# Kernel tuning notes

Hardware: AMD Instinct MI355X
Metric: run time of the kernel (lower is better)

The kernel has to match this reference:

```python
import jax, jax.numpy as jnp
import numpy as np

EPS = 1e-6
ROPE_THETA = 10000.0


def rms_norm(x, w):
    # x: [..., hd]
    var = jnp.mean(x * x, axis=-1, keepdims=True)
    return x * jax.lax.rsqrt(var + EPS) * w


def apply_rope(x):
    # x: [B, L, nH, hd], rotate-half RoPE over sequence positions
    B, L, nH, hd = x.shape
    half = hd // 2
    inv_freq = 1.0 / (ROPE_THETA ** (jnp.arange(half, dtype=jnp.float32) / half))
    pos = jnp.arange(L, dtype=jnp.float32)
    freqs = pos[:, None] * inv_freq[None, :]          # [L, half]
    cos = jnp.cos(freqs)[None, :, None, :]            # [1, L, 1, half]
    sin = jnp.sin(freqs)[None, :, None, :]
    x1, x2 = x[..., :half], x[..., half:]
    return jnp.concatenate([x1 * cos - x2 * sin, x1 * sin + x2 * cos], axis=-1)


def setup_inputs() -> dict:
    key = jax.random.key(0)
    ks = jax.random.split(key, 5)
    B, H, W, C = 2, 48, 48, 512
    nH, nKV = 8, 4
    hd = C // nH
    s = 0.02
    return {
        "x": jax.random.normal(ks[0], (B, H, W, C), jnp.float32),
        "wq": jax.random.normal(ks[1], (C, C), jnp.float32) * s,
        "wk": jax.random.normal(ks[2], (C, nKV * hd), jnp.float32) * s,
        "wv": jax.random.normal(ks[3], (C, nKV * hd), jnp.float32) * s,
        "wo": jax.random.normal(ks[4], (C, C), jnp.float32) * s,
        "q_norm_w": jnp.ones((hd,), jnp.float32),
        "k_norm_w": jnp.ones((hd,), jnp.float32),
    }


def reference(x, wq, wk, wv, wo, q_norm_w, k_norm_w):
    B, H, W, C = x.shape
    L = H * W
    nH = 8
    hd = C // nH
    nKV = wk.shape[-1] // hd

    xf = x.reshape(B, L, C)
    q = (xf @ wq).reshape(B, L, nH, hd)
    k = (xf @ wk).reshape(B, L, nKV, hd)
    v = (xf @ wv).reshape(B, L, nKV, hd)

    q = apply_rope(rms_norm(q, q_norm_w))
    k = apply_rope(rms_norm(k, k_norm_w))

    q = q.transpose(0, 2, 1, 3)                       # [B, nH, L, hd]
    k = k.transpose(0, 2, 1, 3)                       # [B, nKV, L, hd]
    v = v.transpose(0, 2, 1, 3)
    if nKV < nH:
        rep = nH // nKV
        k = jnp.repeat(k, rep, axis=1)                # repeat_interleave over heads
        v = jnp.repeat(v, rep, axis=1)

    scale = 1.0 / jnp.sqrt(jnp.array(hd, jnp.float32))
    scores = jnp.einsum("bhqd,bhkd->bhqk", q, k) * scale
    attn = jax.nn.softmax(scores, axis=-1)
    out = jnp.einsum("bhqk,bhkd->bhqd", attn, v)      # [B, nH, L, hd]
    out = out.transpose(0, 2, 1, 3).reshape(B, H, W, C)
    return out @ wo
```

## Files before the change

### kernel.cpp

```cpp
#include <hip/hip_runtime.h>
#include <cstdint>
#include <cmath>

typedef float    f32x4  __attribute__((ext_vector_type(4)));
typedef uint32_t u32x4  __attribute__((ext_vector_type(4)));
typedef uint16_t u16x8  __attribute__((ext_vector_type(8)));
typedef __bf16   bf16x8 __attribute__((ext_vector_type(8)));

#define DEVI __device__ __forceinline__

#if __has_builtin(__builtin_amdgcn_exp2f)
DEVI float fast_exp2(float x) { return __builtin_amdgcn_exp2f(x); }
#else
DEVI float fast_exp2(float x) { return exp2f(x); }
#endif

constexpr int L   = 2304;
constexpr int C   = 512;
constexpr int NH  = 8;
constexpr int NKV = 4;
constexpr int HD  = 64;
constexpr int Bn  = 2;
constexpr int M   = Bn * L;
constexpr int NQKV = C + 2 * NKV * HD;
constexpr int NSPLIT = 4;
constexpr int KTILES = 36 / NSPLIT;

constexpr int LDP = 72;

DEVI uint16_t f2bf(float f) {
  union { float f; uint32_t u; } v; v.f = f;
  uint32_t u = v.u;
  return (uint16_t)((u + 0x7fffu + ((u >> 16) & 1u)) >> 16);
}
DEVI float bf2f(uint16_t h) {
  union { uint32_t u; float f; } v; v.u = ((uint32_t)h) << 16;
  return v.f;
}
DEVI uint16_t f2h(float f) {
  _Float16 h = (_Float16)f;
  return __builtin_bit_cast(uint16_t, h);
}
DEVI float h2f(uint16_t u) {
  return (float)__builtin_bit_cast(_Float16, u);
}

DEVI bool detect_fp32(const void* qw_raw) {
  return ((const uint16_t*)qw_raw)[0] == 0;
}

DEVI f32x4 mfma_bf16(u32x4 a, u32x4 b, f32x4 c) {
  return __builtin_amdgcn_mfma_f32_16x16x32_bf16(
      __builtin_bit_cast(bf16x8, a), __builtin_bit_cast(bf16x8, b), c, 0, 0, 0);
}

DEVI void gld16(const void* g, void* l) {
  __builtin_amdgcn_global_load_lds((const __attribute__((address_space(1))) void*)g,
                                   (__attribute__((address_space(3))) void*)l,
                                   16, 0, 0);
}

__global__ __launch_bounds__(256) void k_prep(
    const void* __restrict__ x,
    const void* __restrict__ wq, const void* __restrict__ wk,
    const void* __restrict__ wv, const void* __restrict__ wo,
    const void* __restrict__ qw_raw,
    uint16_t* __restrict__ xb,
    uint16_t* __restrict__ wqkvT, uint16_t* __restrict__ woT) {
  const bool f32 = detect_fp32(qw_raw);
  const int bi = blockIdx.x;
  const int t = threadIdx.x;
  if (bi >= 192) {
    const int i = ((bi - 192) * 256 + t) * 8;
    if (f32) {
      const float* xf = (const float*)x;
      const f32x4 v0 = *(const f32x4*)&xf[i];
      const f32x4 v1 = *(const f32x4*)&xf[i + 4];
      u16x8 o;
#pragma unroll
      for (int j = 0; j < 4; ++j) { o[j] = f2bf(v0[j]); o[j + 4] = f2bf(v1[j]); }
      *(u16x8*)&xb[i] = o;
    } else {
      *(u16x8*)&xb[i] = *(const u16x8*)((const uint16_t*)x + i);
    }
    return;
  }
  __shared__ uint16_t tile[64][72];
  const void* src; uint16_t* dst;
  int src_ld, col0, n0, k0;
  if (bi < 128) {
    const int nt = bi & 15, kt = bi >> 4;
    n0 = nt * 64; k0 = kt * 64;
    if (n0 < 512)      { src = wq; src_ld = 512; col0 = n0; }
    else if (n0 < 768) { src = wk; src_ld = 256; col0 = n0 - 512; }
    else               { src = wv; src_ld = 256; col0 = n0 - 768; }
    dst = wqkvT + n0 * 512 + k0;
  } else {
    const int bi2 = bi - 128;
    const int nt = bi2 & 7, kt = bi2 >> 3;
    n0 = nt * 64; k0 = kt * 64;
    src = wo; src_ld = 512; col0 = n0;
    dst = woT + n0 * 512 + k0;
  }
  const int rr = t >> 2, c4 = t & 3;
  if (f32) {
    const float* s32 = (const float*)src;
    for (int cc = c4; cc < 8; cc += 4) {
      const f32x4 v0 = *(const f32x4*)&s32[(k0 + rr) * src_ld + col0 + cc * 8];
      const f32x4 v1 = *(const f32x4*)&s32[(k0 + rr) * src_ld + col0 + cc * 8 + 4];
      for (int j = 0; j < 4; ++j) {
        tile[rr][cc * 8 + j]     = f2bf(v0[j]);
        tile[rr][cc * 8 + j + 4] = f2bf(v1[j]);
      }
    }
  } else {
    const uint16_t* s16 = (const uint16_t*)src;
    for (int cc = c4; cc < 8; cc += 4) {
      const u16x8 v = *(const u16x8*)&s16[(k0 + rr) * src_ld + col0 + cc * 8];
      for (int j = 0; j < 8; ++j) tile[rr][cc * 8 + j] = v[j];
    }
  }
  __syncthreads();
  for (int cc = c4; cc < 8; cc += 4) {
    u16x8 o;
    for (int j = 0; j < 8; ++j) o[j] = tile[cc * 8 + j][rr];
    *(u16x8*)&dst[rr * 512 + cc * 8] = o;
  }
}

DEVI void gemm128_core(const uint16_t* __restrict__ A, const uint16_t* __restrict__ Bt,
                       int m0, int n0, uint16_t* As, uint16_t* Bs, f32x4 acc[4][4]) {
  const int t = threadIdx.x;
  const int lane = t & 63, wave = t >> 6;
  const int l15 = lane & 15, quad = lane >> 4;
  const int wm = wave >> 1, wn = wave & 1;
#pragma unroll
  for (int i = 0; i < 4; ++i)
#pragma unroll
    for (int j = 0; j < 4; ++j) acc[i][j] = f32x4{0.f, 0.f, 0.f, 0.f};

  for (int k0 = 0; k0 < C; k0 += 64) {
    __syncthreads();
#pragma unroll
    for (int rr = 0; rr < 4; ++rr) {
      const int slotbase = rr * 256 + wave * 64;
      const int slot = slotbase + lane;
      const int row = slot >> 3;
      const int ch = (slot & 7) ^ (row & 7);
      gld16(&A [(m0 + row) * C + k0 + ch * 8], &As[slotbase * 8]);
      gld16(&Bt[(n0 + row) * C + k0 + ch * 8], &Bs[slotbase * 8]);
    }
    __syncthreads();
#pragma unroll
    for (int ks = 0; ks < 2; ++ks) {
      const int c = ks * 4 + quad;
      u32x4 af[4], bf[4];
#pragma unroll
      for (int mt = 0; mt < 4; ++mt) {
        const int r = wm * 64 + mt * 16 + l15;
        af[mt] = *(const u32x4*)&As[r * 64 + (c ^ (r & 7)) * 8];
      }
#pragma unroll
      for (int nt = 0; nt < 4; ++nt) {
        const int r = wn * 64 + nt * 16 + l15;
        bf[nt] = *(const u32x4*)&Bs[r * 64 + (c ^ (r & 7)) * 8];
      }
#pragma unroll
      for (int mt = 0; mt < 4; ++mt)
#pragma unroll
        for (int nt = 0; nt < 4; ++nt)
          acc[mt][nt] = mfma_bf16(af[mt], bf[nt], acc[mt][nt]);
    }
  }
}

__global__ __launch_bounds__(256, 2) void k_gemm_qkv(
    const uint16_t* __restrict__ xb, const uint16_t* __restrict__ wqkvT,
    uint16_t* __restrict__ q_p, uint16_t* __restrict__ k_p, uint16_t* __restrict__ v_t,
    const void* __restrict__ qw_raw, const void* __restrict__ kw_raw) {
  __shared__ uint16_t As[128 * 64], Bs[128 * 64];
  const bool f32 = detect_fp32(qw_raw);
  const int m0 = blockIdx.x * 128, n0 = blockIdx.y * 128;
  f32x4 acc[4][4];
  gemm128_core(xb, wqkvT, m0, n0, As, Bs, acc);
  const int t = threadIdx.x, lane = t & 63, wave = t >> 6;
  const int l15 = lane & 15, quad = lane >> 4;
  const int wm = wave >> 1, wn = wave & 1;
  const int col0 = n0 + wn * 64;

  if (col0 < C + NKV * HD) {
    const bool isq = (col0 < C);
    const void* wr = isq ? qw_raw : kw_raw;
    float w4[4];
#pragma unroll
    for (int nt = 0; nt < 4; ++nt)
      w4[nt] = f32 ? ((const float*)wr)[nt * 16 + l15]
                   : bf2f(((const uint16_t*)wr)[nt * 16 + l15]);
    const float cfreq = -0.41524101186092f;
    const float f0 = fast_exp2((float)l15 * cfreq);
    const float f1 = fast_exp2((float)(16 + l15) * cfreq);
    float sF0, cF0, sF1, cF1;
    sincosf(f0, &sF0, &cF0);
    sincosf(f1, &sF1, &cF1);
    const float sc = isq ? 0.125f * 1.44269504088896f : 1.0f;
    const int head = isq ? (col0 >> 6) : ((col0 - C) >> 6);
    uint16_t* plane = isq ? q_p : k_p;
    const int nheads = isq ? NH : NKV;
#pragma unroll
    for (int mt = 0; mt < 4; ++mt) {
      const int gm = m0 + wm * 64 + mt * 16 + quad * 4;
      const int b = gm / L;
      const int l = gm - b * L;
      uint16_t* dst = plane + ((b * nheads + head) * L + l) * HD + l15;
      float s0, c0, s1, c1;
      sincosf((float)l * f0, &s0, &c0);
      sincosf((float)l * f1, &s1, &c1);
#pragma unroll
      for (int r = 0; r < 4; ++r) {
        float x0 = acc[mt][0][r], x1 = acc[mt][1][r];
        float x2 = acc[mt][2][r], x3 = acc[mt][3][r];
        float ss = x0 * x0 + x1 * x1 + x2 * x2 + x3 * x3;
        ss += __shfl_xor(ss, 1, 64); ss += __shfl_xor(ss, 2, 64);
        ss += __shfl_xor(ss, 4, 64); ss += __shfl_xor(ss, 8, 64);
        const float inv = 1.0f / sqrtf(ss * (1.0f / 64.0f) + 1e-6f);
        x0 *= inv * w4[0]; x1 *= inv * w4[1]; x2 *= inv * w4[2]; x3 *= inv * w4[3];
        dst[r * HD +  0] = f2bf((x0 * c0 - x2 * s0) * sc);
        dst[r * HD + 16] = f2bf((x1 * c1 - x3 * s1) * sc);
        dst[r * HD + 32] = f2bf((x0 * s0 + x2 * c0) * sc);
        dst[r * HD + 48] = f2bf((x1 * s1 + x3 * c1) * sc);
        const float ns0 = s0 * cF0 + c0 * sF0, nc0 = c0 * cF0 - s0 * sF0;
        const float ns1 = s1 * cF1 + c1 * sF1, nc1 = c1 * cF1 - s1 * sF1;
        s0 = ns0; c0 = nc0; s1 = ns1; c1 = nc1;
      }
    }
  } else {
    const int vh = (col0 - C - NKV * HD) >> 6;
#pragma unroll
    for (int mt = 0; mt < 4; ++mt) {
      const int gm = m0 + wm * 64 + mt * 16 + quad * 4;
      const int b = gm / L;
      const int l = gm - b * L;
#pragma unroll
      for (int nt = 0; nt < 4; ++nt) {
        uint16_t* dst = v_t + ((b * NKV + vh) * HD + nt * 16 + l15) * L + l;
#pragma unroll
        for (int r = 0; r < 4; ++r) dst[r] = f2bf(acc[mt][nt][r]);
      }
    }
  }
}

__global__ __launch_bounds__(256, 3) void k_attn(
    const uint16_t* __restrict__ q_p, const uint16_t* __restrict__ k_p,
    const uint16_t* __restrict__ v_t,
    uint16_t* __restrict__ Ohat, float* __restrict__ lpart) {
  __shared__ uint16_t Ks[2][4096], Vs[4096];
  __shared__ uint16_t Ps[4][48 * LDP];
  const int t = threadIdx.x, lane = t & 63, wave = t >> 6;
  const int l15 = lane & 15, quad = lane >> 4;

  const int bid = blockIdx.x;
  const int s   = bid / 192;
  const int rem = bid - s * 192;
  const int bkvh = rem / 24;
  const int qg   = rem - bkvh * 24;
  const int b = bkvh >> 2, kvh = bkvh & 3;
  const int u = qg * 4 + wave;
  const int h_local = u / 48;
  const int qt = u - h_local * 48;
  const int bh = b * NH + kvh * 2 + h_local;
  const int q0 = qt * 48;

  const uint16_t* qbase = q_p + (bh * L + q0) * HD;
  const uint16_t* kbase = k_p + (b * NKV + kvh) * L * HD;
  const uint16_t* vbase = v_t + (b * NKV + kvh) * HD * L;
  const int kstart = s * KTILES * 64;

  u32x4 qf[3][2];
#pragma unroll
  for (int mt = 0; mt < 3; ++mt)
#pragma unroll
    for (int ks = 0; ks < 2; ++ks)
      qf[mt][ks] = *(const u32x4*)&qbase[(mt * 16 + l15) * HD + (ks * 4 + quad) * 8];

  f32x4 O[3][4];
  float lp[3][4];
#pragma unroll
  for (int mt = 0; mt < 3; ++mt) {
#pragma unroll
    for (int nt = 0; nt < 4; ++nt) O[mt][nt] = f32x4{0.f, 0.f, 0.f, 0.f};
#pragma unroll
    for (int r = 0; r < 4; ++r) lp[mt][r] = 0.f;
  }

  uint16_t* Pw = Ps[wave];

  auto stageK = [&](int key0, int buf) {
#pragma unroll
    for (int rr = 0; rr < 2; ++rr) {
      const int slotbase = rr * 256 + wave * 64;
      const int slot = slotbase + lane;
      const int row = slot >> 3, cs = slot & 7;
      const int ch = cs ^ (row & 7);
      gld16(&kbase[(key0 + row) * HD + ch * 8], &Ks[buf][slotbase * 8]);
    }
  };
  auto stageV = [&](int key0) {
#pragma unroll
    for (int rr = 0; rr < 2; ++rr) {
      const int slotbase = rr * 256 + wave * 64;
      const int slot = slotbase + lane;
      const int row = slot >> 3, cs = slot & 7;
      const int ch = cs ^ (row & 7);
      gld16(&vbase[row * L + key0 + ch * 8], &Vs[slotbase * 8]);
    }
  };

  stageK(kstart, 0);

#pragma unroll 1
  for (int kb = 0; kb < KTILES; ++kb) {
    const int cur = kb & 1;
    __syncthreads();
    stageV(kstart + kb * 64);
    if (kb + 1 < KTILES) stageK(kstart + (kb + 1) * 64, cur ^ 1);

#pragma unroll
    for (int nt = 0; nt < 4; ++nt) {
      f32x4 S[3];
#pragma unroll
      for (int mt = 0; mt < 3; ++mt) S[mt] = f32x4{0.f, 0.f, 0.f, 0.f};
      const int kr = nt * 16 + l15;
#pragma unroll
      for (int ks = 0; ks < 2; ++ks) {
        const int ch = ks * 4 + quad;
        const u32x4 kf = *(const u32x4*)&Ks[cur][(kr * 8 + (ch ^ (kr & 7))) * 8];
        __builtin_amdgcn_s_setprio(1);
#pragma unroll
        for (int mt = 0; mt < 3; ++mt)
          S[mt] = mfma_bf16(qf[mt][ks], kf, S[mt]);
        __builtin_amdgcn_s_setprio(0);
      }
#pragma unroll
      for (int mt = 0; mt < 3; ++mt)
#pragma unroll
        for (int r = 0; r < 4; ++r) {
          const float p = fast_exp2(S[mt][r]);
          lp[mt][r] += p;
          Pw[(mt * 16 + quad * 4 + r) * LDP + nt * 16 + l15] = f2bf(p);
        }
    }

    __syncthreads();

#pragma unroll
    for (int ks = 0; ks < 2; ++ks) {
      const int ch = ks * 4 + quad;
      u32x4 pf[3];
#pragma unroll
      for (int mt = 0; mt < 3; ++mt)
        pf[mt] = *(const u32x4*)&Pw[(mt * 16 + l15) * LDP + ch * 8];
#pragma unroll
      for (int nt = 0; nt < 4; ++nt) {
        const int dr = nt * 16 + l15;
        const u32x4 vf = *(const u32x4*)&Vs[(dr * 8 + (ch ^ (dr & 7))) * 8];
        __builtin_amdgcn_s_setprio(1);
#pragma unroll
        for (int mt = 0; mt < 3; ++mt)
          O[mt][nt] = mfma_bf16(pf[mt], vf, O[mt][nt]);
        __builtin_amdgcn_s_setprio(0);
      }
    }
  }

  const int obase = (s * 16 + bh) * L + q0;
#pragma unroll
  for (int mt = 0; mt < 3; ++mt)
#pragma unroll
    for (int r = 0; r < 4; ++r) {
      float lv = lp[mt][r];
#pragma unroll
      for (int m = 1; m < 16; m <<= 1) lv += __shfl_xor(lv, m, 64);
      const float rl = 1.0f / lv;
      const int row = obase + mt * 16 + quad * 4 + r;
      if (l15 == 0) lpart[row] = lv;
#pragma unroll
      for (int nt = 0; nt < 4; ++nt)
        Ohat[row * HD + nt * 16 + l15] = f2h(O[mt][nt][r] * rl);
    }
}

__global__ __launch_bounds__(256) void k_combine(
    const uint16_t* __restrict__ Ohat, const float* __restrict__ lpart,
    uint16_t* __restrict__ attn) {
  const int idx8 = blockIdx.x * 256 + threadIdx.x;
  const int row = idx8 >> 3, d0 = (idx8 & 7) * 8;
  float o[8] = {0.f, 0.f, 0.f, 0.f, 0.f, 0.f, 0.f, 0.f};
  float l = 0.f;
#pragma unroll
  for (int s = 0; s < NSPLIT; ++s) {
    const float ls = lpart[s * 16 * L + row];
    const u16x8 v = *(const u16x8*)&Ohat[(s * 16 * L + row) * HD + d0];
#pragma unroll
    for (int j = 0; j < 8; ++j) o[j] += h2f(v[j]) * ls;
    l += ls;
  }
  const int bh = row / L, lq = row - bh * L;
  const int b = bh >> 3, h = bh & 7;
  const float rl = 1.0f / l;
  u16x8 ov;
#pragma unroll
  for (int j = 0; j < 8; ++j) ov[j] = f2bf(o[j] * rl);
  *(u16x8*)&attn[(b * L + lq) * C + h * HD + d0] = ov;
}

__global__ __launch_bounds__(256, 2) void k_gemm_out(
    const uint16_t* __restrict__ attn, const uint16_t* __restrict__ woT,
    void* __restrict__ out, const void* __restrict__ qw_raw) {
  __shared__ uint16_t As[128 * 64], Bs[128 * 64];
  const bool f32 = detect_fp32(qw_raw);
  const int m0 = blockIdx.x * 128, n0 = blockIdx.y * 128;
  f32x4 acc[4][4];
  gemm128_core(attn, woT, m0, n0, As, Bs, acc);
  const int t = threadIdx.x, lane = t & 63, wave = t >> 6;
  const int l15 = lane & 15, quad = lane >> 4;
  const int wm = wave >> 1, wn = wave & 1;
#pragma unroll
  for (int mt = 0; mt < 4; ++mt) {
    const int gm = m0 + wm * 64 + mt * 16 + quad * 4;
#pragma unroll
    for (int nt = 0; nt < 4; ++nt) {
      const int gn = n0 + wn * 64 + nt * 16 + l15;
      if (f32) {
        float* o32 = (float*)out;
#pragma unroll
        for (int r = 0; r < 4; ++r) o32[(gm + r) * C + gn] = acc[mt][nt][r];
      } else {
        uint16_t* o16 = (uint16_t*)out;
#pragma unroll
        for (int r = 0; r < 4; ++r) o16[(gm + r) * C + gn] = f2bf(acc[mt][nt][r]);
      }
    }
  }
}

extern "C" void kernel_launch(void* const* d_in, const int* in_sizes, int n_in,
                              void* d_out, int out_size, void* d_ws, size_t ws_size,
                              hipStream_t stream) {
  const void* x  = d_in[0];
  const void* wq = d_in[1];
  const void* wk = d_in[2];
  const void* wv = d_in[3];
  const void* wo = d_in[4];
  const void* qw = d_in[5];
  const void* kw = d_in[6];

  uint16_t* ws = (uint16_t*)d_ws;
  uint16_t* xb    = ws;
  uint16_t* wqkvT = xb    + M * C;
  uint16_t* woT   = wqkvT + 1024 * 512;
  uint16_t* q_p   = woT   + 512 * 512;
  uint16_t* k_p   = q_p + Bn * NH  * L * HD;
  uint16_t* v_t   = k_p + Bn * NKV * L * HD;
  uint16_t* attn  = v_t + Bn * NKV * L * HD;
  uint16_t* Ohat  = attn + M * C;
  float*    lpart = (float*)(Ohat + NSPLIT * 16 * L * HD);

  k_prep      <<<dim3(192 + M * C / (256 * 8)), dim3(256), 0, stream>>>(
                  x, wq, wk, wv, wo, qw, xb, wqkvT, woT);
  k_gemm_qkv  <<<dim3(M / 128, NQKV / 128), dim3(256), 0, stream>>>(
                  xb, wqkvT, q_p, k_p, v_t, qw, kw);
  k_attn      <<<dim3(768), dim3(256), 0, stream>>>(q_p, k_p, v_t, Ohat, lpart);
  k_combine   <<<dim3(16 * L * HD / (256 * 8)), dim3(256), 0, stream>>>(Ohat, lpart, attn);
  k_gemm_out  <<<dim3(M / 128, C / 128), dim3(256), 0, stream>>>(attn, woT, d_out, qw);
}
```

Before: 139.7 us.

## Keep attention probabilities in registers via transposed S and permlane swaps

The QK^T MFMA is computed transposed (K as A operand) so each lane holds probabilities along the key dimension. They are packed to bf16 with v_cvt_pk_bf16_f32 and rearranged with permlane32/16 swaps into the A-operand layout for the PV MFMA. This removes the per-wave LDS staging buffer for P and its store/load traffic, and also simplifies the row-sum reduction. The cost is extra register pressure and reliance on gfx950-specific permlane instructions, with correctness depending on the lane mapping.

New measurement: 134.5 us. -3.7%, faster.

```diff
diff --git a/kernel.cpp b/kernel.cpp
--- a/kernel.cpp
+++ b/kernel.cpp
@@ -26,8 +26,6 @@
 constexpr int NSPLIT = 4;
 constexpr int KTILES = 36 / NSPLIT;
 
-constexpr int LDP = 72;
-
 DEVI uint16_t f2bf(float f) {
   union { float f; uint32_t u; } v; v.f = f;
   uint32_t u = v.u;
@@ -52,6 +50,18 @@
 DEVI f32x4 mfma_bf16(u32x4 a, u32x4 b, f32x4 c) {
   return __builtin_amdgcn_mfma_f32_16x16x32_bf16(
       __builtin_bit_cast(bf16x8, a), __builtin_bit_cast(bf16x8, b), c, 0, 0, 0);
+}
+
+DEVI uint32_t cvt_pk_bf16(float a, float b) {
+  uint32_t r;
+  asm("v_cvt_pk_bf16_f32 %0, %1, %2" : "=v"(r) : "v"(a), "v"(b));
+  return r;
+}
+DEVI void permlane32_swap(uint32_t& a, uint32_t& b) {
+  asm("v_permlane32_swap_b32 %0, %1" : "+v"(a), "+v"(b));
+}
+DEVI void permlane16_swap(uint32_t& a, uint32_t& b) {
+  asm("v_permlane16_swap_b32 %0, %1" : "+v"(a), "+v"(b));
 }
 
 DEVI void gld16(const void* g, void* l) {
@@ -255,7 +265,6 @@
     const uint16_t* __restrict__ v_t,
     uint16_t* __restrict__ Ohat, float* __restrict__ lpart) {
   __shared__ uint16_t Ks[2][4096], Vs[4096];
-  __shared__ uint16_t Ps[4][48 * LDP];
   const int t = threadIdx.x, lane = t & 63, wave = t >> 6;
   const int l15 = lane & 15, quad = lane >> 4;
 
@@ -284,16 +293,13 @@
       qf[mt][ks] = *(const u32x4*)&qbase[(mt * 16 + l15) * HD + (ks * 4 + quad) * 8];
 
   f32x4 O[3][4];
-  float lp[3][4];
+  float lp[3];
 #pragma unroll
   for (int mt = 0; mt < 3; ++mt) {
 #pragma unroll
     for (int nt = 0; nt < 4; ++nt) O[mt][nt] = f32x4{0.f, 0.f, 0.f, 0.f};
-#pragma unroll
-    for (int r = 0; r < 4; ++r) lp[mt][r] = 0.f;
-  }
-
-  uint16_t* Pw = Ps[wave];
+    lp[mt] = 0.f;
+  }
 
   auto stageK = [&](int key0, int buf) {
 #pragma unroll
@@ -325,49 +331,67 @@
     stageV(kstart + kb * 64);
     if (kb + 1 < KTILES) stageK(kstart + (kb + 1) * 64, cur ^ 1);
 
-#pragma unroll
-    for (int nt = 0; nt < 4; ++nt) {
-      f32x4 S[3];
-#pragma unroll
-      for (int mt = 0; mt < 3; ++mt) S[mt] = f32x4{0.f, 0.f, 0.f, 0.f};
-      const int kr = nt * 16 + l15;
-#pragma unroll
-      for (int ks = 0; ks < 2; ++ks) {
-        const int ch = ks * 4 + quad;
-        const u32x4 kf = *(const u32x4*)&Ks[cur][(kr * 8 + (ch ^ (kr & 7))) * 8];
-        __builtin_amdgcn_s_setprio(1);
-#pragma unroll
-        for (int mt = 0; mt < 3; ++mt)
-          S[mt] = mfma_bf16(qf[mt][ks], kf, S[mt]);
-        __builtin_amdgcn_s_setprio(0);
-      }
+    u32x4 pa[3][2];
+
+#pragma unroll
+    for (int ntp = 0; ntp < 2; ++ntp) {
+      f32x4 S[2][3];
+#pragma unroll
+      for (int ntl = 0; ntl < 2; ++ntl)
+#pragma unroll
+        for (int mt = 0; mt < 3; ++mt) S[ntl][mt] = f32x4{0.f, 0.f, 0.f, 0.f};
+#pragma unroll
+      for (int ntl = 0; ntl < 2; ++ntl) {
+        const int kr = (ntp * 2 + ntl) * 16 + l15;
+#pragma unroll
+        for (int dks = 0; dks < 2; ++dks) {
+          const int ch = dks * 4 + quad;
+          const u32x4 kf = *(const u32x4*)&Ks[cur][(kr * 8 + (ch ^ (kr & 7))) * 8];
+          __builtin_amdgcn_s_setprio(1);
+#pragma unroll
+          for (int mt = 0; mt < 3; ++mt)
+            S[ntl][mt] = mfma_bf16(kf, qf[mt][dks], S[ntl][mt]);
+          __builtin_amdgcn_s_setprio(0);
+        }
+      }
+      uint32_t P32[2][3][2];
+#pragma unroll
+      for (int ntl = 0; ntl < 2; ++ntl)
+#pragma unroll
+        for (int mt = 0; mt < 3; ++mt) {
+          const float p0 = fast_exp2(S[ntl][mt][0]);
+          const float p1 = fast_exp2(S[ntl][mt][1]);
+          const float p2 = fast_exp2(S[ntl][mt][2]);
+          const float p3 = fast_exp2(S[ntl][mt][3]);
+          lp[mt] += (p0 + p1) + (p2 + p3);
+          P32[ntl][mt][0] = cvt_pk_bf16(p0, p1);
+          P32[ntl][mt][1] = cvt_pk_bf16(p2, p3);
+        }
 #pragma unroll
       for (int mt = 0; mt < 3; ++mt)
 #pragma unroll
-        for (int r = 0; r < 4; ++r) {
-          const float p = fast_exp2(S[mt][r]);
-          lp[mt][r] += p;
-          Pw[(mt * 16 + quad * 4 + r) * LDP + nt * 16 + l15] = f2bf(p);
+        for (int j2 = 0; j2 < 2; ++j2) {
+          uint32_t x = P32[0][mt][j2], y = P32[1][mt][j2];
+          permlane32_swap(x, y);
+          permlane16_swap(x, y);
+          pa[mt][ntp][j2]     = x;
+          pa[mt][ntp][2 + j2] = y;
         }
     }
 
     __syncthreads();
 
 #pragma unroll
-    for (int ks = 0; ks < 2; ++ks) {
-      const int ch = ks * 4 + quad;
-      u32x4 pf[3];
-#pragma unroll
-      for (int mt = 0; mt < 3; ++mt)
-        pf[mt] = *(const u32x4*)&Pw[(mt * 16 + l15) * LDP + ch * 8];
+    for (int pks = 0; pks < 2; ++pks) {
 #pragma unroll
       for (int nt = 0; nt < 4; ++nt) {
         const int dr = nt * 16 + l15;
+        const int ch = pks * 4 + quad;
         const u32x4 vf = *(const u32x4*)&Vs[(dr * 8 + (ch ^ (dr & 7))) * 8];
         __builtin_amdgcn_s_setprio(1);
 #pragma unroll
         for (int mt = 0; mt < 3; ++mt)
-          O[mt][nt] = mfma_bf16(pf[mt], vf, O[mt][nt]);
+          O[mt][nt] = mfma_bf16(pa[mt][pks], vf, O[mt][nt]);
         __builtin_amdgcn_s_setprio(0);
       }
     }
@@ -375,19 +399,20 @@
 
   const int obase = (s * 16 + bh) * L + q0;
 #pragma unroll
-  for (int mt = 0; mt < 3; ++mt)
+  for (int mt = 0; mt < 3; ++mt) {
+    float lv = lp[mt];
+    lv += __shfl_xor(lv, 16, 64);
+    lv += __shfl_xor(lv, 32, 64);
+    if (lane < 16) lpart[obase + mt * 16 + lane] = lv;
 #pragma unroll
     for (int r = 0; r < 4; ++r) {
-      float lv = lp[mt][r];
-#pragma unroll
-      for (int m = 1; m < 16; m <<= 1) lv += __shfl_xor(lv, m, 64);
-      const float rl = 1.0f / lv;
+      const float rl = 1.0f / __shfl(lv, quad * 4 + r, 64);
       const int row = obase + mt * 16 + quad * 4 + r;
-      if (l15 == 0) lpart[row] = lv;
 #pragma unroll
       for (int nt = 0; nt < 4; ++nt)
         Ohat[row * HD + nt * 16 + l15] = f2h(O[mt][nt][r] * rl);
     }
+  }
 }
 
 __global__ __launch_bounds__(256) void k_combine(
```
